# Kernel optimization log

Measured on AMD Instinct MI355X. Metric: run time of the kernel, lower is better.

Reference implementation:

```python
import jax, jax.numpy as jnp
import numpy as np
from jax import lax

B, C, H, W = 2, 64, 128, 128
NBR, G, K, P, CK = 4, 8, 3, 11, 3
PAD = 6  # (CK-1)//2 + (P-1)//2


def conv2d(x, w, b, pad):
    y = lax.conv_general_dilated(x, w, (1, 1), [(pad, pad), (pad, pad)],
                                 dimension_numbers=('NCHW', 'OIHW', 'NCHW'))
    return y + b[None, :, None, None]


def l2norm(x):
    n = jnp.sqrt(jnp.sum(x * x, axis=1, keepdims=True))
    return x / jnp.maximum(n, 1e-12)


def correlation(f1, f2):
    # spatial correlation sampler: kernel=3, patch=11, stride=1, padding=1
    # corr[b, ph*11+pw, h, w] = sum_{c,ki,kj} f1[b,c,h+ki-1,w+kj-1]*f2[b,c,h+ki-1+ph-5,w+kj-1+pw-5]
    f1p = jnp.pad(f1, ((0, 0), (0, 0), (1, 1), (1, 1)))
    f2p = jnp.pad(f2, ((0, 0), (0, 0), (PAD, PAD), (PAD, PAD)))
    offs = jnp.array([(ph, pw) for ph in range(P) for pw in range(P)], dtype=jnp.int32)

    def one(off):
        sl = lax.dynamic_slice(f2p, (0, 0, off[0], off[1]), (B, C, H + 2, W + 2))
        q = jnp.einsum('bchw,bchw->bhw', f1p, sl)  # (B,H+2,W+2)
        # 3x3 box sum -> (B,H,W)
        return sum(q[:, ki:ki + H, kj:kj + W] for ki in range(CK) for kj in range(CK))

    corr = lax.map(one, offs)  # (121,B,H,W)
    return jnp.transpose(corr, (1, 0, 2, 3))  # (B,121,H,W)


def setup_inputs() -> dict:
    key = jax.random.key(0)
    ks = jax.random.split(key, 12)
    s = 0.05
    return {
        'nbr_fea': jax.random.normal(ks[0], (B, C, H, W), jnp.float32),
        'ref_fea': jax.random.normal(ks[1], (B, C, H, W), jnp.float32),
        'conv1_w': jax.random.normal(ks[2], (C, 2 * C, 3, 3), jnp.float32) * s,
        'conv1_b': jax.random.normal(ks[3], (C,), jnp.float32) * s,
        'conv2_w': jax.random.normal(ks[4], (C, C, 3, 3), jnp.float32) * s,
        'conv2_b': jax.random.normal(ks[5], (C,), jnp.float32) * s,
        'mask_w': jax.random.normal(ks[6], (G * K * K, C, K, K), jnp.float32) * s,
        'mask_b': jax.random.normal(ks[7], (G * K * K,), jnp.float32) * s,
        'nn_w': jax.random.normal(ks[8], (C, NBR * C, 3, 3), jnp.float32) * s,
        'nn_b': jax.random.normal(ks[9], (C,), jnp.float32) * s,
        'agg_w': jax.random.normal(ks[10], (C, 2 * C, 3, 3), jnp.float32) * s,
        'agg_b': jax.random.normal(ks[11], (C,), jnp.float32) * s,
    }


def reference(nbr_fea, ref_fea, conv1_w, conv1_b, conv2_w, conv2_b,
              mask_w, mask_b, nn_w, nn_b, agg_w, agg_b):
    # mask branch
    wf = conv2d(jnp.concatenate([nbr_fea, ref_fea], axis=1), conv1_w, conv1_b, 1)
    wf = conv2d(wf, conv2_w, conv2_b, 1)
    mask = conv2d(wf, mask_w, mask_b, (K - 1) // 2).reshape(B, G, 1, K * K, H, W)

    # local correlation + topk neighbor selection
    corr = correlation(l2norm(ref_fea), l2norm(nbr_fea))  # (B,121,H,W)
    idx = lax.top_k(jnp.transpose(corr, (0, 2, 3, 1)), NBR)[1]  # (B,H,W,NBR)
    ph, pw = idx // P, idx % P

    # gather 3x3 patches centered at displacement (ph-5, pw-5) from pad-6 nbr features
    nbr_pad = jnp.pad(nbr_fea, ((0, 0), (0, 0), (PAD, PAD), (PAD, PAD)))
    r0 = jnp.arange(H)[None, :, None, None] + ph  # (B,H,W,NBR) top-left row in padded img
    c0 = jnp.arange(W)[None, None, :, None] + pw
    ki = jnp.arange(CK)

    def gather_b(fp, r, c):
        R = r[..., None, None] + ki[:, None]   # (H,W,NBR,3,1)
        Cc = c[..., None, None] + ki[None, :]  # (H,W,NBR,1,3)
        return fp[:, R, Cc]  # (C,H,W,NBR,3,3)

    patches = jax.vmap(gather_b)(nbr_pad, r0, c0)  # (B,C,H,W,NBR,3,3)
    L = jnp.transpose(patches, (0, 2, 3, 4, 1, 5, 6)).reshape(B * H * W, NBR * C, CK, CK)
    L = conv2d(L, nn_w, nn_b, 1)  # (B*H*W, C, 3, 3)
    L = L.reshape(B, H, W, C, CK * CK)
    L = jnp.transpose(L, (0, 3, 4, 1, 2)).reshape(B, G, C // G, CK * CK, H, W)

    agg = jnp.sum(L * mask, axis=3).reshape(B, C, H, W)
    agg = jnp.where(agg >= 0, agg, 0.1 * agg)  # LeakyReLU(0.1)
    out = conv2d(jnp.concatenate([agg, ref_fea], axis=1), agg_w, agg_b, 1)
    return out
```

## Files before the change

kernel.cpp:

```cpp
#include <hip/hip_runtime.h>
#include <hip/hip_bf16.h>
#include <math.h>

#define HH 128
#define WW 128
#define HWSZ 16384

typedef __attribute__((ext_vector_type(8))) short short8;
typedef __attribute__((ext_vector_type(4))) float f32x4;

constexpr int OFF_CATT  = 0;
constexpr int OFF_CAT2T = 8388608;
constexpr int OFF_WF1   = 16777216;
constexpr int OFF_WF2   = 20971520;
constexpr int OFF_MASK  = 25165824;
constexpr int OFF_IDX   = 34603008;
constexpr int OFF_WT1   = 35127296;
constexpr int OFF_WT2   = 35274752;
constexpr int OFF_WTM   = 35348480;
constexpr int OFF_WTA   = 35495936;
constexpr int OFF_ZROW  = 35643392;
constexpr int OFF_WB    = 35644416;
constexpr int OFF_F1T   = 38797312;
constexpr int OFF_F2T   = 47185920;
constexpr int OFF_D     = 55574528;
constexpr int OFF_PV    = 71434240;
constexpr int OFF_PP    = 77201408;

__device__ inline ushort f2bf(float f) {
    __hip_bfloat16 h = __float2bfloat16(f);
    return *reinterpret_cast<ushort*>(&h);
}
__device__ inline float bf2f(ushort u) {
    return __uint_as_float(((unsigned)u) << 16);
}

__device__ inline void gload16(const void* g, void* l) {
    __builtin_amdgcn_global_load_lds(
        (const __attribute__((address_space(1))) unsigned int*)g,
        (__attribute__((address_space(3))) unsigned int*)l, 16, 0, 0);
}

__device__ void l2t2_body(int bid, const float* __restrict__ in,
                          float4* __restrict__ normT4,
                          ushort* __restrict__ d1, ushort* __restrict__ d2)
{
    const int pix0 = bid * 64;
    const int b = pix0 >> 14;
    const int hw0 = pix0 & (HWSZ - 1);
    __shared__ float s[64][65];
    __shared__ float sinv[64];
    const int tid = threadIdx.x;
    {
        const int p = tid & 63, c4 = tid >> 6;
#pragma unroll
        for (int r = 0; r < 16; ++r) {
            int c = r * 4 + c4;
            s[c][p] = in[(((size_t)b * 64 + c) << 14) + hw0 + p];
        }
    }
    __syncthreads();
    if (tid < 64) {
        float sum = 0.f;
#pragma unroll
        for (int c = 0; c < 64; ++c) { float v = s[c][tid]; sum = fmaf(v, v, sum); }
        sinv[tid] = 1.f / fmaxf(sqrtf(sum), 1e-12f);
    }
    __syncthreads();
    {
        const int pp = tid & 63, cg = tid >> 6;
        const float inv = sinv[pp];
#pragma unroll
        for (int r = 0; r < 4; ++r) {
            int c4 = cg * 4 + r;
            float4 v = make_float4(s[c4 * 4 + 0][pp] * inv, s[c4 * 4 + 1][pp] * inv,
                                   s[c4 * 4 + 2][pp] * inv, s[c4 * 4 + 3][pp] * inv);
            normT4[(((size_t)b * 16 + c4) << 14) + hw0 + pp] = v;
        }
    }
    {
        const int c = tid & 63, p4 = tid >> 6;
#pragma unroll
        for (int r = 0; r < 16; ++r) {
            int pp = r * 4 + p4;
            ushort bv = f2bf(s[c][pp]);
            d1[(size_t)(pix0 + pp) * 128 + c] = bv;
            if (d2) d2[(size_t)(pix0 + pp) * 128 + c] = bv;
        }
    }
}

__device__ inline ushort wt_elem(const float* __restrict__ w, int Cin, int Cout, int idx) {
    int kc = 9 * Cin;
    int o = idx / kc, rem = idx % kc;
    int tap = rem / Cin, c = rem % Cin;
    float val = (o < Cout) ? w[((size_t)o * Cin + c) * 9 + tap] : 0.f;
    return f2bf(val);
}

__device__ void prep_body(int bid,
                          const float* __restrict__ c1w, const float* __restrict__ c2w,
                          const float* __restrict__ mw,  const float* __restrict__ aw,
                          const float* __restrict__ nnw, char* __restrict__ W)
{
    int gid = bid * 256 + threadIdx.x;
    if (gid < 73728) {
        ((ushort*)(W + OFF_WT1))[gid] = wt_elem(c1w, 128, 64, gid);
    } else if (gid < 110592) {
        int i = gid - 73728;
        ((ushort*)(W + OFF_WT2))[i] = wt_elem(c2w, 64, 64, i);
    } else if (gid < 165888) {
        int i = gid - 110592;
        ((ushort*)(W + OFF_WTM))[i] = wt_elem(mw, 64, 72, i);
    } else if (gid < 239616) {
        int i = gid - 165888;
        ((ushort*)(W + OFF_WTA))[i] = wt_elem(aw, 128, 64, i);
    } else if (gid < 387072) {
        int idx = gid - 239616;
        int j = idx / 36864, rem = idx % 36864;
        int rb = rem >> 6, c = rem & 63;
        int e = rb >> 6, o = rb & 63;
        int ky = e / 3, kx = e % 3;
        ((ushort*)(W + OFF_WB))[idx] =
            f2bf(nnw[(((size_t)o * 256 + j * 64 + c) * 3 + ky) * 3 + kx]);
    } else if (gid < 387200) {
        ((ushort*)(W + OFF_ZROW))[gid - 387072] = 0;
    }
}

__device__ void dot_body(int bid, const float4* __restrict__ f1t4,
                         const float4* __restrict__ f2t4, float* __restrict__ D)
{
    const int pix = (bid & 127) * 256 + threadIdx.x;
    const int q = bid >> 7;
    const int b = pix >> 14, hw = pix & (HWSZ - 1), h = hw >> 7, w = hw & 127;
    const int y = h + q - 5;
    float* Dq = D + ((((size_t)b * 121) + q * 11) << 14) + hw;

    if ((unsigned)y >= (unsigned)HH) {
#pragma unroll
        for (int pw = 0; pw < 11; ++pw) Dq[(size_t)pw << 14] = 0.f;
        return;
    }
    float acc[11] = {};
    const float4* f1p  = f1t4 + (((size_t)b * 16) << 14) + hw;
    const float4* rowb = f2t4 + (((size_t)b * 16) << 14) + (y << 7);

#pragma unroll 4
    for (int c4 = 0; c4 < 16; ++c4) {
        float4 a = f1p[(size_t)c4 << 14];
        const float4* rp = rowb + ((size_t)c4 << 14);
#pragma unroll
        for (int pw = 0; pw < 11; ++pw) {
            int x = w + pw - 5;
            if ((unsigned)x < (unsigned)WW) {
                float4 c = rp[x];
                acc[pw] = fmaf(a.x, c.x, acc[pw]);
                acc[pw] = fmaf(a.y, c.y, acc[pw]);
                acc[pw] = fmaf(a.z, c.z, acc[pw]);
                acc[pw] = fmaf(a.w, c.w, acc[pw]);
            }
        }
    }
#pragma unroll
    for (int pw = 0; pw < 11; ++pw) Dq[(size_t)pw << 14] = acc[pw];
}

__device__ void topk_s1_body(int bid, const float* __restrict__ D,
                             float4* __restrict__ Pv, int4* __restrict__ Pp)
{
    const int pix = (bid & 127) * 256 + threadIdx.x;
    const int q = bid >> 7;
    const int b = pix >> 14, hw = pix & (HWSZ - 1), h = hw >> 7, w = hw & 127;
    const int lane = threadIdx.x & 63;
    const float* Db = D + (((size_t)b * 121) << 14);

    float bv[4] = {-1e30f, -1e30f, -1e30f, -1e30f};
    int   bi[4] = {1 << 20, 1 << 20, 1 << 20, 1 << 20};

    for (int pw = 0; pw < 11; ++pw) {
        const int p = q * 11 + pw;
        const float* Dp = Db + ((size_t)p << 14);
        float v = 0.f, vx = 0.f;
#pragma unroll
        for (int dy = -1; dy <= 1; ++dy) {
            int y = h + dy;
            if ((unsigned)y < HH) {
                v += Dp[(y << 7) + w];
                if (lane == 0) { if (w > 0) vx += Dp[(y << 7) + w - 1]; }
                else if (lane == 63) { if (w < 127) vx += Dp[(y << 7) + w + 1]; }
            }
        }
        float vl = __shfl_up(v, 1);
        float vr = __shfl_down(v, 1);
        if (lane == 0)  vl = (w > 0)   ? vx : 0.f;
        if (lane == 63) vr = (w < 127) ? vx : 0.f;
        float s = vl + v + vr;
        if (s > bv[3]) {
            if (s > bv[0]) { bv[3]=bv[2];bi[3]=bi[2]; bv[2]=bv[1];bi[2]=bi[1]; bv[1]=bv[0];bi[1]=bi[0]; bv[0]=s; bi[0]=p; }
            else if (s > bv[1]) { bv[3]=bv[2];bi[3]=bi[2]; bv[2]=bv[1];bi[2]=bi[1]; bv[1]=s; bi[1]=p; }
            else if (s > bv[2]) { bv[3]=bv[2];bi[3]=bi[2]; bv[2]=s; bi[2]=p; }
            else { bv[3]=s; bi[3]=p; }
        }
    }
    Pv[(size_t)q * 32768 + pix] = make_float4(bv[0], bv[1], bv[2], bv[3]);
    Pp[(size_t)q * 32768 + pix] = make_int4(bi[0], bi[1], bi[2], bi[3]);
}

__device__ void topk_s2_body(int bid, const float4* __restrict__ Pv,
                             const int4* __restrict__ Pp, int* __restrict__ idxout)
{
    const int pix = bid * 256 + threadIdx.x;
    float bv2[4] = {-1e30f, -1e30f, -1e30f, -1e30f};
    int   bi2[4] = {1 << 20, 1 << 20, 1 << 20, 1 << 20};
    for (int qq = 0; qq < 11; ++qq) {
        float4 v4 = Pv[(size_t)qq * 32768 + pix];
        int4   p4 = Pp[(size_t)qq * 32768 + pix];
        float vv[4] = {v4.x, v4.y, v4.z, v4.w};
        int   pp4[4] = {p4.x, p4.y, p4.z, p4.w};
#pragma unroll
        for (int r = 0; r < 4; ++r) {
            float v = vv[r]; int pp = pp4[r];
            bool g3 = (v > bv2[3]) || (v == bv2[3] && pp < bi2[3]);
            if (g3) {
                bool g0 = (v > bv2[0]) || (v == bv2[0] && pp < bi2[0]);
                bool g1 = (v > bv2[1]) || (v == bv2[1] && pp < bi2[1]);
                bool g2 = (v > bv2[2]) || (v == bv2[2] && pp < bi2[2]);
                if (g0) { bv2[3]=bv2[2];bi2[3]=bi2[2]; bv2[2]=bv2[1];bi2[2]=bi2[1]; bv2[1]=bv2[0];bi2[1]=bi2[0]; bv2[0]=v; bi2[0]=pp; }
                else if (g1) { bv2[3]=bv2[2];bi2[3]=bi2[2]; bv2[2]=bv2[1];bi2[2]=bi2[1]; bv2[1]=v; bi2[1]=pp; }
                else if (g2) { bv2[3]=bv2[2];bi2[3]=bi2[2]; bv2[2]=v; bi2[2]=pp; }
                else { bv2[3]=v; bi2[3]=pp; }
            }
        }
    }
    int p0 = (bi2[0] / 11) | ((bi2[0] % 11) << 16);
    int p1 = (bi2[1] / 11) | ((bi2[1] % 11) << 16);
    int p2 = (bi2[2] / 11) | ((bi2[2] % 11) << 16);
    int p3 = (bi2[3] / 11) | ((bi2[3] % 11) << 16);
    ((int4*)idxout)[pix] = make_int4(p0, p1, p2, p3);
}

template<int CINPT, int OUTFMT, int BM, int BN, int WN>
__device__ void mmconv_body(int by,
    const char* __restrict__ Wb, int src_off, int rowbytes, int zoff,
    const ushort* __restrict__ WT, int Ktot,
    const float* __restrict__ bias,
    void* __restrict__ outp, int ostride, int nvalid)
{
    constexpr int WM = 4 / WN;
    constexpr int FM = BM / (WM * 16);
    constexpr int FN = BN / (WN * 16);
    constexpr int NA = BM / 32;
    constexpr int NB = BN / 32;
    const int n0 = 0;
    const int m0 = by * BM;
    const int tid = threadIdx.x;
    const int lane = tid & 63, wv = tid >> 6;
    const int lr = lane >> 4, lc = lane & 15;
    const int wr = wv / WN, wc = wv % WN;

    __shared__ __align__(16) char sA[2][BM * 128];
    __shared__ __align__(16) char sB[2][BN * 128];

    int hA[NA], wA[NA], aBase[NA], swzA[NA];
#pragma unroll
    for (int i = 0; i < NA; ++i) {
        int r  = (i * 4 + wv) * 8 + (lane >> 3);
        int pm = m0 + r;
        int hw = pm & (HWSZ - 1);
        hA[i] = hw >> 7; wA[i] = hw & 127;
        aBase[i] = src_off + (pm >> 14) * (HWSZ * rowbytes);
        swzA[i]  = ((lane & 7) ^ (r & 7)) << 4;
    }
    int boff[NB];
#pragma unroll
    for (int i = 0; i < NB; ++i) {
        int rb = (i * 4 + wv) * 8 + (lane >> 3);
        boff[i] = (n0 + rb) * Ktot * 2 + (((lane & 7) ^ (rb & 7)) << 4);
    }

    f32x4 acc[FM][FN] = {};
    const int NST = Ktot / 64;

#define CSTAGE(S, B)                                                             \
    {                                                                            \
        int k0 = (S) * 64;                                                       \
        int tap = k0 / CINPT;                                                    \
        int c0b = (k0 % CINPT) * 2;                                              \
        int du = tap / 3 - 1, dv = tap % 3 - 1;                                  \
        _Pragma("unroll")                                                        \
        for (int i = 0; i < NA; ++i) {                                           \
            int y = hA[i] + du, x = wA[i] + dv;                                  \
            bool ok = ((unsigned)y < (unsigned)HH) && ((unsigned)x < (unsigned)WW); \
            int off = ok ? (aBase[i] + ((y << 7) + x) * rowbytes + c0b + swzA[i]) : zoff; \
            gload16(Wb + (unsigned)off, &sA[(B)][(i * 4 + wv) * 1024]);          \
        }                                                                        \
        _Pragma("unroll")                                                        \
        for (int i = 0; i < NB; ++i)                                             \
            gload16((const char*)WT + (unsigned)(boff[i] + (S) * 128),           \
                    &sB[(B)][(i * 4 + wv) * 1024]);                              \
    }

    CSTAGE(0, 0)
    __syncthreads();
#pragma unroll 1
    for (int s = 0; s < NST; ++s) {
        if (s + 1 < NST) { CSTAGE(s + 1, (s + 1) & 1) }
        const char* cA = sA[s & 1];
        const char* cB = sB[s & 1];
#pragma unroll
        for (int ks = 0; ks < 2; ++ks) {
            short8 af[FM]; short8 bfr[FN];
            const int u = ks * 4 + lr;
#pragma unroll
            for (int f = 0; f < FM; ++f) {
                int rr = wr * (FM * 16) + f * 16 + lc;
                af[f] = *(const short8*)&cA[rr * 128 + ((u ^ (rr & 7)) << 4)];
            }
#pragma unroll
            for (int g = 0; g < FN; ++g) {
                int nn = wc * (FN * 16) + g * 16 + lc;
                bfr[g] = *(const short8*)&cB[nn * 128 + ((u ^ (nn & 7)) << 4)];
            }
#pragma unroll
            for (int f = 0; f < FM; ++f)
#pragma unroll
                for (int g = 0; g < FN; ++g)
                    acc[f][g] = __builtin_amdgcn_mfma_f32_16x16x32_bf16(af[f], bfr[g], acc[f][g], 0, 0, 0);
        }
        __syncthreads();
    }
#undef CSTAGE

#pragma unroll
    for (int f = 0; f < FM; ++f)
#pragma unroll
        for (int g = 0; g < FN; ++g) {
            const int col = n0 + wc * (FN * 16) + g * 16 + lc;
            float bv = (bias != nullptr && col < nvalid) ? bias[col] : 0.f;
            if (OUTFMT == 2) {
                const int mb = m0 + wr * (FM * 16) + f * 16 + lr * 4;
                const int bb = mb >> 14, hww = mb & (HWSZ - 1);
                float4 o4 = {acc[f][g][0] + bv, acc[f][g][1] + bv,
                             acc[f][g][2] + bv, acc[f][g][3] + bv};
                *(float4*)((float*)outp + (((size_t)(bb * 64 + col)) << 14) + hww) = o4;
            } else {
#pragma unroll
                for (int reg = 0; reg < 4; ++reg) {
                    const int m = m0 + wr * (FM * 16) + f * 16 + lr * 4 + reg;
                    float v = acc[f][g][reg] + bv;
                    if (OUTFMT == 0)
                        ((ushort*)outp)[(size_t)m * ostride + col] = f2bf(v);
                    else if (col < nvalid)
                        ((float*)outp)[(size_t)m * ostride + col] = v;
                }
            }
        }
}

__global__ __launch_bounds__(256) void k0_prep_l2t2(
    const float* __restrict__ ref, const float* __restrict__ nbr,
    const float* __restrict__ c1w, const float* __restrict__ c2w,
    const float* __restrict__ mw,  const float* __restrict__ aw,
    const float* __restrict__ nnw, char* __restrict__ W)
{
    const int bid = blockIdx.x;
    if (bid < 512) {
        l2t2_body(bid, ref, (float4*)(W + OFF_F1T),
                  (ushort*)(W + OFF_CATT) + 64, (ushort*)(W + OFF_CAT2T) + 64);
    } else if (bid < 1024) {
        l2t2_body(bid - 512, nbr, (float4*)(W + OFF_F2T),
                  (ushort*)(W + OFF_CATT), (ushort*)nullptr);
    } else {
        prep_body(bid - 1024, c1w, c2w, mw, aw, nnw, W);
    }
}

__global__ __launch_bounds__(256) void k1_conv1_dot(
    char* __restrict__ W, const float* __restrict__ c1b)
{
    const int bid = blockIdx.x;
    if (bid < 1024) {
        mmconv_body<128, 0, 32, 64, 4>(bid, W, OFF_CATT, 256, OFF_ZROW,
            (ushort*)(W + OFF_WT1), 1152, c1b, W + OFF_WF1, 64, 64);
    } else {
        dot_body(bid - 1024, (const float4*)(W + OFF_F1T),
                 (const float4*)(W + OFF_F2T), (float*)(W + OFF_D));
    }
}

__global__ __launch_bounds__(256) void k2_conv2_s1(
    char* __restrict__ W, const float* __restrict__ c2b)
{
    const int bid = blockIdx.x;
    if (bid < 1024) {
        mmconv_body<64, 0, 32, 64, 4>(bid, W, OFF_WF1, 128, OFF_ZROW,
            (ushort*)(W + OFF_WT2), 576, c2b, W + OFF_WF2, 64, 64);
    } else {
        topk_s1_body(bid - 1024, (const float*)(W + OFF_D),
                     (float4*)(W + OFF_PV), (int4*)(W + OFF_PP));
    }
}

__global__ __launch_bounds__(256) void k3_convM_s2(
    char* __restrict__ W, const float* __restrict__ mb)
{
    const int bid = blockIdx.x;
    if (bid < 1024) {
        mmconv_body<64, 1, 32, 96, 2>(bid, W, OFF_WF2, 128, OFF_ZROW,
            (ushort*)(W + OFF_WTM), 576, mb, (float*)(W + OFF_MASK), 72, 72);
    } else {
        topk_s2_body(bid - 1024, (const float4*)(W + OFF_PV),
                     (const int4*)(W + OFF_PP), (int*)(W + OFF_IDX));
    }
}

__global__ __launch_bounds__(256) void convA_kernel(
    char* __restrict__ W, const float* __restrict__ ab, float* __restrict__ out)
{
    mmconv_body<128, 2, 32, 64, 4>(blockIdx.x, W, OFF_CAT2T, 256, OFF_ZROW,
        (ushort*)(W + OFF_WTA), 1152, ab, out, 0, 64);
}

__global__ __launch_bounds__(256, 2) void patch_kernel(
    const char* __restrict__ Wb, int cat_off, int idx_off, int zoff, int wb_off,
    const float* __restrict__ maskcl, const float* __restrict__ nnb,
    ushort* __restrict__ aggout)
{
    const int m0 = blockIdx.x * 32;
    const int tid = threadIdx.x;
    const int lane = tid & 63, wv = tid >> 6;
    const int lr = lane >> 4, lc = lane & 15;
    const int wr = wv >> 1, wc = wv & 1;

    __shared__ __align__(16) char sP[36864 + 2 * 16384];

    const int r    = tid >> 3;
    const int pm_s = m0 + r;
    const int hw_s = pm_s & (HWSZ - 1);
    const int hS = hw_s >> 7, wS = hw_s & 127;
    const int aBase = cat_off + (pm_s >> 14) * (HWSZ * 256);
    const int swzA  = ((tid & 7) ^ (r & 7)) << 4;
    int bsrc[2];
#pragma unroll
    for (int i = 0; i < 2; ++i) {
        int rl = i * 32 + r;
        bsrc[i] = wb_off + rl * 128 + (((tid & 7) ^ (rl & 7)) << 4);
    }
    const int* idxr = (const int*)(Wb + idx_off);

    f32x4 acc[9][2] = {};

#pragma unroll 1
    for (int j = 0; j < 4; ++j) {
        const int pk = idxr[pm_s * 4 + j];
        const int hp = hS + (pk & 0xffff) - 6;
        const int wp = wS + (pk >> 16) - 6;

        __syncthreads();
#pragma unroll
        for (int uv = 0; uv < 9; ++uv) {
            int y = hp + uv / 3, x = wp + uv % 3;
            bool ok = ((unsigned)y < (unsigned)HH) && ((unsigned)x < (unsigned)WW);
            int off = ok ? (aBase + ((y << 7) + x) * 256 + swzA) : zoff;
            gload16(Wb + (unsigned)off, &sP[uv * 4096 + wv * 1024]);
        }
#pragma unroll
        for (int eg = 0; eg < 2; ++eg)
#pragma unroll
            for (int i = 0; i < 2; ++i)
                gload16(Wb + (unsigned)(bsrc[i] + j * 73728 + eg * 8192),
                        &sP[36864 + eg * 8192 + i * 4096 + wv * 1024]);
        __syncthreads();

        short8 af[9][2];
#pragma unroll
        for (int uv = 0; uv < 9; ++uv)
#pragma unroll
            for (int ks = 0; ks < 2; ++ks) {
                const int rr = wr * 16 + lc;
                af[uv][ks] = *(const short8*)&sP[uv * 4096 + rr * 128 +
                                                (((ks * 4 + lr) ^ (rr & 7)) << 4)];
            }

#pragma unroll
        for (int g = 0; g < 5; ++g) {
            if (g < 4) {
                const int nslot = (g + 1) & 1;
#pragma unroll
                for (int eg = 0; eg < 2; ++eg) {
                    const int ne = 2 * (g + 1) + eg;
                    if (ne > 8) continue;
#pragma unroll
                    for (int i = 0; i < 2; ++i)
                        gload16(Wb + (unsigned)(bsrc[i] + j * 73728 + ne * 8192),
                                &sP[36864 + nslot * 16384 + eg * 8192 + i * 4096 + wv * 1024]);
                }
            }
#pragma unroll
            for (int eg = 0; eg < 2; ++eg) {
                const int e = 2 * g + eg;
                if (e > 8) continue;
                const char* bt = &sP[36864 + (g & 1) * 16384 + eg * 8192];
                short8 bfr[2][2];
#pragma unroll
                for (int gg = 0; gg < 2; ++gg) {
                    const int rloc = wc * 32 + gg * 16 + lc;
#pragma unroll
                    for (int ks = 0; ks < 2; ++ks)
                        bfr[gg][ks] = *(const short8*)&bt[rloc * 128 +
                                                          (((ks * 4 + lr) ^ (rloc & 7)) << 4)];
                }
                const int ky = e / 3, kx = e % 3;
#pragma unroll
                for (int uv = 0; uv < 9; ++uv) {
                    const int uu = uv / 3, vv = uv % 3;
                    const int ty = uu - ky + 1, tx = vv - kx + 1;
                    if (ty < 0 || ty > 2 || tx < 0 || tx > 2) continue;
                    const int t = ty * 3 + tx;
#pragma unroll
                    for (int gg = 0; gg < 2; ++gg) {
                        acc[t][gg] = __builtin_amdgcn_mfma_f32_16x16x32_bf16(af[uv][0], bfr[gg][0], acc[t][gg], 0, 0, 0);
                        acc[t][gg] = __builtin_amdgcn_mfma_f32_16x16x32_bf16(af[uv][1], bfr[gg][1], acc[t][gg], 0, 0, 0);
                    }
                }
            }
            if (g < 4) __syncthreads();
        }
    }

#pragma unroll
    for (int gg = 0; gg < 2; ++gg) {
        const int col_o = wc * 32 + gg * 16 + lc;
        const float bo = nnb[col_o];
        const int og = col_o >> 3;
#pragma unroll
        for (int reg = 0; reg < 4; ++reg) {
            const int m = m0 + wr * 16 + lr * 4 + reg;
            const float* mp = maskcl + (size_t)m * 72 + og * 9;
            float s = 0.f;
#pragma unroll
            for (int t = 0; t < 9; ++t) s += (acc[t][gg][reg] + bo) * mp[t];
            s = (s >= 0.f) ? s : 0.1f * s;
            aggout[(size_t)m * 128 + col_o] = f2bf(s);
        }
    }
}

extern "C" void kernel_launch(void* const* d_in, const int* in_sizes, int n_in,
                              void* d_out, int out_size, void* d_ws, size_t ws_size,
                              hipStream_t stream)
{
    const float* nbr = (const float*)d_in[0];
    const float* ref = (const float*)d_in[1];
    const float* c1w = (const float*)d_in[2];
    const float* c1b = (const float*)d_in[3];
    const float* c2w = (const float*)d_in[4];
    const float* c2b = (const float*)d_in[5];
    const float* mw  = (const float*)d_in[6];
    const float* mb  = (const float*)d_in[7];
    const float* nnw = (const float*)d_in[8];
    const float* nnb = (const float*)d_in[9];
    const float* aw  = (const float*)d_in[10];
    const float* ab  = (const float*)d_in[11];
    float* out = (float*)d_out;

    char* W = (char*)d_ws;
    dim3 blk(256);

    k0_prep_l2t2<<<2537, blk, 0, stream>>>(ref, nbr, c1w, c2w, mw, aw, nnw, W);

    k1_conv1_dot<<<2432, blk, 0, stream>>>(W, c1b);

    k2_conv2_s1<<<2432, blk, 0, stream>>>(W, c2b);

    k3_convM_s2<<<1152, blk, 0, stream>>>(W, mb);

    patch_kernel<<<1024, blk, 0, stream>>>(W, OFF_CATT, OFF_IDX, OFF_ZROW, OFF_WB,
                                           (const float*)(W + OFF_MASK), nnb,
                                           (ushort*)(W + OFF_CAT2T));

    convA_kernel<<<1024, blk, 0, stream>>>(W, ab, out);
}
```

Before: 164.8 us.

## Compute two pixels per thread in correlation dot and pipeline patch-kernel loads across neighbors

```diff
diff --git a/kernel.cpp b/kernel.cpp
--- a/kernel.cpp
+++ b/kernel.cpp
@@ -128,42 +128,57 @@
     }
 }
 
-__device__ void dot_body(int bid, const float4* __restrict__ f1t4,
-                         const float4* __restrict__ f2t4, float* __restrict__ D)
-{
-    const int pix = (bid & 127) * 256 + threadIdx.x;
-    const int q = bid >> 7;
-    const int b = pix >> 14, hw = pix & (HWSZ - 1), h = hw >> 7, w = hw & 127;
+__device__ void dot_body2(int bid, const float4* __restrict__ f1t4,
+                          const float4* __restrict__ f2t4, float* __restrict__ D)
+{
+    const int q = bid >> 6;
+    const int pix0 = ((bid & 63) << 9) + (threadIdx.x << 1);
+    const int b = pix0 >> 14, hw = pix0 & (HWSZ - 1), h = hw >> 7, w = hw & 127;
     const int y = h + q - 5;
     float* Dq = D + ((((size_t)b * 121) + q * 11) << 14) + hw;
 
     if ((unsigned)y >= (unsigned)HH) {
 #pragma unroll
-        for (int pw = 0; pw < 11; ++pw) Dq[(size_t)pw << 14] = 0.f;
+        for (int pw = 0; pw < 11; ++pw)
+            *(float2*)&Dq[(size_t)pw << 14] = make_float2(0.f, 0.f);
         return;
     }
-    float acc[11] = {};
+    float acc[11][2] = {};
     const float4* f1p  = f1t4 + (((size_t)b * 16) << 14) + hw;
     const float4* rowb = f2t4 + (((size_t)b * 16) << 14) + (y << 7);
 
-#pragma unroll 4
+#pragma unroll 2
     for (int c4 = 0; c4 < 16; ++c4) {
-        float4 a = f1p[(size_t)c4 << 14];
+        float4 a0 = f1p[(size_t)c4 << 14];
+        float4 a1 = f1p[((size_t)c4 << 14) + 1];
         const float4* rp = rowb + ((size_t)c4 << 14);
+        float4 f2w[12];
+#pragma unroll
+        for (int k = 0; k < 12; ++k) {
+            int x = w - 5 + k;
+            f2w[k] = ((unsigned)x < (unsigned)WW) ? rp[x] : make_float4(0.f, 0.f, 0.f, 0.f);
+        }
 #pragma unroll
         for (int pw = 0; pw < 11; ++pw) {
-            int x = w + pw - 5;
-            if ((unsigned)x < (unsigned)WW) {
-                float4 c = rp[x];
-                acc[pw] = fmaf(a.x, c.x, acc[pw]);
-                acc[pw] = fmaf(a.y, c.y, acc[pw]);
-                acc[pw] = fmaf(a.z, c.z, acc[pw]);
-                acc[pw] = fmaf(a.w, c.w, acc[pw]);
-            }
-        }
-    }
-#pragma unroll
-    for (int pw = 0; pw < 11; ++pw) Dq[(size_t)pw << 14] = acc[pw];
+            {
+                float4 c = f2w[pw];
+                acc[pw][0] = fmaf(a0.x, c.x, acc[pw][0]);
+                acc[pw][0] = fmaf(a0.y, c.y, acc[pw][0]);
+                acc[pw][0] = fmaf(a0.z, c.z, acc[pw][0]);
+                acc[pw][0] = fmaf(a0.w, c.w, acc[pw][0]);
+            }
+            {
+                float4 c = f2w[pw + 1];
+                acc[pw][1] = fmaf(a1.x, c.x, acc[pw][1]);
+                acc[pw][1] = fmaf(a1.y, c.y, acc[pw][1]);
+                acc[pw][1] = fmaf(a1.z, c.z, acc[pw][1]);
+                acc[pw][1] = fmaf(a1.w, c.w, acc[pw][1]);
+            }
+        }
+    }
+#pragma unroll
+    for (int pw = 0; pw < 11; ++pw)
+        *(float2*)&Dq[(size_t)pw << 14] = make_float2(acc[pw][0], acc[pw][1]);
 }
 
 __device__ void topk_s1_body(int bid, const float* __restrict__ D,
@@ -384,8 +399,8 @@
         mmconv_body<128, 0, 32, 64, 4>(bid, W, OFF_CATT, 256, OFF_ZROW,
             (ushort*)(W + OFF_WT1), 1152, c1b, W + OFF_WF1, 64, 64);
     } else {
-        dot_body(bid - 1024, (const float4*)(W + OFF_F1T),
-                 (const float4*)(W + OFF_F2T), (float*)(W + OFF_D));
+        dot_body2(bid - 1024, (const float4*)(W + OFF_F1T),
+                  (const float4*)(W + OFF_F2T), (float*)(W + OFF_D));
     }
 }
 
@@ -447,32 +462,41 @@
         int rl = i * 32 + r;
         bsrc[i] = wb_off + rl * 128 + (((tid & 7) ^ (rl & 7)) << 4);
     }
-    const int* idxr = (const int*)(Wb + idx_off);
+    const int4 pk4 = ((const int4*)(Wb + idx_off))[pm_s];
 
     f32x4 acc[9][2] = {};
+
+#define ISSUE_A(PK)                                                              \
+    {                                                                            \
+        const int hp = hS + ((PK) & 0xffff) - 6;                                 \
+        const int wp = wS + ((PK) >> 16) - 6;                                    \
+        _Pragma("unroll")                                                        \
+        for (int uv = 0; uv < 9; ++uv) {                                         \
+            int y = hp + uv / 3, x = wp + uv % 3;                                \
+            bool ok = ((unsigned)y < (unsigned)HH) && ((unsigned)x < (unsigned)WW); \
+            int off = ok ? (aBase + ((y << 7) + x) * 256 + swzA) : zoff;         \
+            gload16(Wb + (unsigned)off, &sP[uv * 4096 + wv * 1024]);             \
+        }                                                                        \
+    }
+#define ISSUE_B(J, G, SLOT)                                                      \
+    {                                                                            \
+        _Pragma("unroll")                                                        \
+        for (int eg = 0; eg < 2; ++eg) {                                         \
+            const int ne = 2 * (G) + eg;                                         \
+            if (ne > 8) continue;                                                \
+            _Pragma("unroll")                                                    \
+            for (int i = 0; i < 2; ++i)                                          \
+                gload16(Wb + (unsigned)(bsrc[i] + (J) * 73728 + ne * 8192),      \
+                        &sP[36864 + (SLOT) * 16384 + eg * 8192 + i * 4096 + wv * 1024]); \
+        }                                                                        \
+    }
+
+    ISSUE_A(pk4.x)
+    ISSUE_B(0, 0, 0)
+    __syncthreads();
 
 #pragma unroll 1
     for (int j = 0; j < 4; ++j) {
-        const int pk = idxr[pm_s * 4 + j];
-        const int hp = hS + (pk & 0xffff) - 6;
-        const int wp = wS + (pk >> 16) - 6;
-
-        __syncthreads();
-#pragma unroll
-        for (int uv = 0; uv < 9; ++uv) {
-            int y = hp + uv / 3, x = wp + uv % 3;
-            bool ok = ((unsigned)y < (unsigned)HH) && ((unsigned)x < (unsigned)WW);
-            int off = ok ? (aBase + ((y << 7) + x) * 256 + swzA) : zoff;
-            gload16(Wb + (unsigned)off, &sP[uv * 4096 + wv * 1024]);
-        }
-#pragma unroll
-        for (int eg = 0; eg < 2; ++eg)
-#pragma unroll
-            for (int i = 0; i < 2; ++i)
-                gload16(Wb + (unsigned)(bsrc[i] + j * 73728 + eg * 8192),
-                        &sP[36864 + eg * 8192 + i * 4096 + wv * 1024]);
-        __syncthreads();
-
         short8 af[9][2];
 #pragma unroll
         for (int uv = 0; uv < 9; ++uv)
@@ -485,23 +509,19 @@
 
 #pragma unroll
         for (int g = 0; g < 5; ++g) {
-            if (g < 4) {
-                const int nslot = (g + 1) & 1;
-#pragma unroll
-                for (int eg = 0; eg < 2; ++eg) {
-                    const int ne = 2 * (g + 1) + eg;
-                    if (ne > 8) continue;
-#pragma unroll
-                    for (int i = 0; i < 2; ++i)
-                        gload16(Wb + (unsigned)(bsrc[i] + j * 73728 + ne * 8192),
-                                &sP[36864 + nslot * 16384 + eg * 8192 + i * 4096 + wv * 1024]);
-                }
-            }
+            const int slot = (j + g) & 1;
+            if (g == 1 && j < 3) {
+                const int pkn = (j == 0) ? pk4.y : (j == 1) ? pk4.z : pk4.w;
+                ISSUE_A(pkn)
+            }
+            if (g < 4) { ISSUE_B(j, g + 1, (j + g + 1) & 1) }
+            else if (j < 3) { ISSUE_B(j + 1, 0, (j + 1) & 1) }
+
 #pragma unroll
             for (int eg = 0; eg < 2; ++eg) {
                 const int e = 2 * g + eg;
                 if (e > 8) continue;
-                const char* bt = &sP[36864 + (g & 1) * 16384 + eg * 8192];
+                const char* bt = &sP[36864 + slot * 16384 + eg * 8192];
                 short8 bfr[2][2];
 #pragma unroll
                 for (int gg = 0; gg < 2; ++gg) {
@@ -525,9 +545,11 @@
                     }
                 }
             }
-            if (g < 4) __syncthreads();
-        }
-    }
+            __syncthreads();
+        }
+    }
+#undef ISSUE_A
+#undef ISSUE_B
 
 #pragma unroll
     for (int gg = 0; gg < 2; ++gg) {
@@ -570,7 +592,7 @@
 
     k0_prep_l2t2<<<2537, blk, 0, stream>>>(ref, nbr, c1w, c2w, mw, aw, nnw, W);
 
-    k1_conv1_dot<<<2432, blk, 0, stream>>>(W, c1b);
+    k1_conv1_dot<<<1728, blk, 0, stream>>>(W, c1b);
 
     k2_conv2_s1<<<2432, blk, 0, stream>>>(W, c2b);
 
```

Measured after the change: 183.2 us. +11.2%, slower.
